# Performance work log

Hardware: AMD Instinct MI355X
Metric: run time of the kernel (lower is better)

## Reference

```python
import jax, jax.numpy as jnp
import numpy as np

N = 100000   # nodes
E = 1600000  # edges
D_IN = 4
D_H = 128
EPS = 1e-5

def setup_inputs() -> dict:
    key = jax.random.key(0)
    ks = jax.random.split(key, 4)
    x = jax.random.normal(ks[0], (N, D_IN), dtype=jnp.float32)
    edge_index = jax.random.randint(ks[1], (2, E), 0, N, dtype=jnp.int32)
    W0 = jax.random.normal(ks[2], (D_IN, D_H), dtype=jnp.float32) * 0.5
    b0 = jnp.zeros((D_H,), jnp.float32)
    W12 = jax.random.normal(ks[3], (2, D_H, D_H), dtype=jnp.float32) * (1.0 / np.sqrt(D_H))
    b12 = jnp.zeros((2, D_H), jnp.float32)
    gamma = jnp.ones((3, D_H), jnp.float32)   # GraphNorm weight
    beta = jnp.zeros((3, D_H), jnp.float32)   # GraphNorm bias
    alpha = jnp.ones((3, D_H), jnp.float32)   # GraphNorm mean_scale
    return dict(x=x, edge_index=edge_index, W0=W0, b0=b0, W12=W12, b12=b12,
                gamma=gamma, beta=beta, alpha=alpha)

def gcn_conv(x, src, dst, dinv, W, b):
    # PyG GCNConv: linear first, then D^-1/2 (A+I) D^-1/2 aggregation, bias after.
    h = x @ W                                  # [N, d_out]
    coef = dinv[src] * dinv[dst]               # [E]
    msg = h[src] * coef[:, None]               # [E, d_out] gather
    agg = jax.ops.segment_sum(msg, dst, num_segments=N)  # scatter-add
    agg = agg + h * (dinv * dinv)[:, None]     # self-loop contribution
    return agg + b

def graph_norm(x, g, be, a):
    # single-graph GraphNorm: gamma*(x - alpha*mu)/sqrt(E[(x-alpha*mu)^2]+eps)+beta
    mu = x.mean(axis=0)
    xc = x - a * mu
    var = (xc * xc).mean(axis=0)
    return g * xc * jax.lax.rsqrt(var + EPS) + be

def reference(x, edge_index, W0, b0, W12, b12, gamma, beta, alpha):
    src, dst = edge_index[0], edge_index[1]
    # degree with self loops (edge weight 1)
    deg = jax.ops.segment_sum(jnp.ones((E,), x.dtype), dst, num_segments=N) + 1.0
    dinv = jax.lax.rsqrt(deg)
    h = jax.nn.relu(graph_norm(gcn_conv(x, src, dst, dinv, W0, b0),
                               gamma[0], beta[0], alpha[0]))
    for i in range(2):  # fixed small layer loop
        h = jax.nn.relu(graph_norm(gcn_conv(h, src, dst, dinv, W12[i], b12[i]),
                                   gamma[i + 1], beta[i + 1], alpha[i + 1]))
    return h
```

## Files before the change

kernel.cpp:

```cpp
#include <hip/hip_runtime.h>


#define EPS_GN 1e-5f

typedef __attribute__((ext_vector_type(8))) _Float16 f16x8;
typedef __attribute__((ext_vector_type(2))) _Float16 f16x2;
typedef __attribute__((ext_vector_type(4))) float f32x4;

template <typename T, typename U>
__device__ __forceinline__ T bc(U u) {
  return __builtin_bit_cast(T, u);
}
__device__ __forceinline__ unsigned pkh(float x, float y) {
  return bc<unsigned>(__builtin_amdgcn_cvt_pkrtz(x, y));
}


__global__ __launch_bounds__(256) void k_count_p(const int* __restrict__ dst,
                                                 int* __restrict__ cnt, int E, int N) {
  int p = blockIdx.x & 7;
  int lo = (int)((long long)N * p >> 3), hi = (int)((long long)N * (p + 1) >> 3);
  int stride = (gridDim.x >> 3) * 256;
  for (int e = (blockIdx.x >> 3) * 256 + threadIdx.x; e < E; e += stride) {
    int d = dst[e];
    if (d >= lo && d < hi) atomicAdd(&cnt[d], 1);
  }
}

__global__ __launch_bounds__(256) void k_scan1(const int* __restrict__ cnt,
                                               int* __restrict__ rs,
                                               int* __restrict__ bsum, int N) {
  __shared__ int s[256];
  int t = threadIdx.x;
  int base = blockIdx.x * 1024 + t * 4;
  int c0 = (base + 0 < N) ? ((cnt[base + 0] + 8) & ~7) : 0;
  int c1 = (base + 1 < N) ? ((cnt[base + 1] + 8) & ~7) : 0;
  int c2 = (base + 2 < N) ? ((cnt[base + 2] + 8) & ~7) : 0;
  int c3 = (base + 3 < N) ? ((cnt[base + 3] + 8) & ~7) : 0;
  int tsum = c0 + c1 + c2 + c3;
  s[t] = tsum;
  __syncthreads();
  for (int off = 1; off < 256; off <<= 1) {
    int v = (t >= off) ? s[t - off] : 0;
    __syncthreads();
    s[t] += v;
    __syncthreads();
  }
  int excl = s[t] - tsum;
  if (t == 255) bsum[blockIdx.x] = s[255];
  int e0 = excl, e1 = e0 + c0, e2 = e1 + c1, e3 = e2 + c2;
  if (base + 0 < N) rs[base + 0] = e0;
  if (base + 1 < N) rs[base + 1] = e1;
  if (base + 2 < N) rs[base + 2] = e2;
  if (base + 3 < N) rs[base + 3] = e3;
}

__global__ __launch_bounds__(256) void k_scan2(const int* __restrict__ bsum,
                                               int* __restrict__ boff, int nblk) {
  __shared__ int s[256];
  int t = threadIdx.x;
  int v0 = (t < nblk) ? bsum[t] : 0;
  s[t] = v0;
  __syncthreads();
  for (int off = 1; off < 256; off <<= 1) {
    int v = (t >= off) ? s[t - off] : 0;
    __syncthreads();
    s[t] += v;
    __syncthreads();
  }
  if (t < nblk) boff[t] = s[t] - v0;
}

__global__ __launch_bounds__(256) void k_finalize(const int* __restrict__ cnt,
                                                  const int* __restrict__ boff,
                                                  int* __restrict__ rs,
                                                  int* __restrict__ cursor,
                                                  float* __restrict__ dinv,
                                                  unsigned* __restrict__ Hcb,
                                                  int* __restrict__ csrp, int N, int E,
                                                  int ROWS) {
  __shared__ int sTail;
  int i = blockIdx.x * 256 + threadIdx.x;
  int NB = N * 32;
  if (i < 64) Hcb[((size_t)(i >> 3) * ROWS + N) * 8 + (i & 7)] = 0u;
  if (i < N) {
    int v = rs[i] + boff[i >> 10];
    int c = cnt[i];
    int pc = (c + 8) & ~7;
    rs[i] = v;
    cursor[i] = v + 1;
    dinv[i] = rsqrtf((float)c + 1.0f);
    csrp[v] = i * 32;
    for (int k = v + 1 + c; k < v + pc; ++k) csrp[k] = NB;
    if (i == N - 1) {
      rs[N] = v + pc;
      sTail = v + pc;
    }
  }
  __syncthreads();
  if (blockIdx.x == gridDim.x - 1) {
    int base = sTail;
    for (int k = threadIdx.x; k < 1024; k += 256) csrp[base + k] = NB;
  }
}

__global__ __launch_bounds__(256) void k_fill_p(const int* __restrict__ src,
                                                const int* __restrict__ dst,
                                                int* __restrict__ cursor,
                                                int* __restrict__ csrp, int E, int N) {
  int p = blockIdx.x & 7;
  int lo = (int)((long long)N * p >> 3), hi = (int)((long long)N * (p + 1) >> 3);
  int stride = (gridDim.x >> 3) * 256;
  for (int e = (blockIdx.x >> 3) * 256 + threadIdx.x; e < E; e += stride) {
    int d = dst[e];
    if (d >= lo && d < hi) {
      int pos = atomicAdd(&cursor[d], 1);
      csrp[pos] = src[e] << 5;
    }
  }
}


__global__ __launch_bounds__(256) void k_wt(const float* __restrict__ W12,
                                            _Float16* __restrict__ WbT) {
  int o = blockIdx.x * 256 + threadIdx.x;
  int layer = o >> 14, r = o & 16383;
  int n = r >> 7, k = r & 127;
  WbT[o] = (_Float16)W12[layer * 16384 + k * 128 + n];
}


__global__ __launch_bounds__(256) void k_gemm0(const float* __restrict__ X,
                                               const float* __restrict__ W,
                                               const float* __restrict__ dinv,
                                               unsigned* __restrict__ Hcb, int N, int ROWS) {
  __shared__ float Ws[4 * 128];
  int t = threadIdx.x;
  if (t < 128) {
    Ws[t] = W[t];
    Ws[128 + t] = W[128 + t];
    Ws[256 + t] = W[256 + t];
    Ws[384 + t] = W[384 + t];
  }
  __syncthreads();
  int r = t >> 6, l = t & 63;
  int row = blockIdx.x * 4 + r;
  if (row >= N) return;
  float4 xv = ((const float4*)X)[row];
  float di = dinv[row];
  int c0 = 2 * l, c1 = 2 * l + 1;
  float v0 = xv.x * Ws[c0] + xv.y * Ws[128 + c0] + xv.z * Ws[256 + c0] + xv.w * Ws[384 + c0];
  float v1 = xv.x * Ws[c1] + xv.y * Ws[128 + c1] + xv.z * Ws[256 + c1] + xv.w * Ws[384 + c1];
  Hcb[((size_t)(l >> 3) * ROWS + row) * 8 + (l & 7)] = pkh(di * v0, di * v1);
}

__global__ __launch_bounds__(256, 4) void k_gemm_mfma(const unsigned* __restrict__ AGGcb,
                                                      const _Float16* __restrict__ WbT,
                                                      const float* __restrict__ stats,
                                                      const float* __restrict__ bias,
                                                      const float* __restrict__ gamma,
                                                      const float* __restrict__ beta,
                                                      const float* __restrict__ alpha,
                                                      const float* __restrict__ dinv,
                                                      unsigned* __restrict__ Hcb, int N,
                                                      int ROWS, float invN) {
  __shared__ float As[128], Bs[128];
  int t = threadIdx.x;
  if (t < 128) {
    float s1 = stats[t] * invN, s2 = stats[128 + t] * invN;
    float b = bias[t], a = alpha[t], g = gamma[t], be = beta[t];
    float mu = s1 + b;
    float E2 = s2 + 2.f * b * s1 + b * b;
    float var = E2 - (2.f * a - a * a) * mu * mu;
    float A = g * rsqrtf(var + EPS_GN);
    As[t] = A;
    Bs[t] = be - A * a * mu + A * b;
  }
  __syncthreads();
  int wv = t >> 6, l = t & 63;
  int r0 = blockIdx.x * 64 + wv * 16;
  if (r0 >= N) return;
  int m = l & 15, kb = l >> 4;

  f32x4 acc[8];
#pragma unroll
  for (int nt = 0; nt < 8; ++nt) acc[nt] = (f32x4){0.f, 0.f, 0.f, 0.f};

#pragma unroll
  for (int ks = 0; ks < 4; ++ks) {
    int k0 = ks * 32 + kb * 8;
    const uint4* pa = (const uint4*)(AGGcb + ((size_t)(2 * ks + (kb >> 1)) * ROWS + r0 + m) * 8 +
                                     (kb & 1) * 4);
    uint4 a_raw = pa[0];
    float4 A0 = *reinterpret_cast<const float4*>(&As[k0]);
    float4 A1 = *reinterpret_cast<const float4*>(&As[k0 + 4]);
    float4 B0 = *reinterpret_cast<const float4*>(&Bs[k0]);
    float4 B1 = *reinterpret_cast<const float4*>(&Bs[k0 + 4]);
    f16x8 bf[8];
#pragma unroll
    for (int nt = 0; nt < 8; ++nt)
      bf[nt] = *reinterpret_cast<const f16x8*>(WbT + (size_t)(nt * 16 + m) * 128 + k0);
    unsigned uu[4] = {a_raw.x, a_raw.y, a_raw.z, a_raw.w};
    float xr[8];
#pragma unroll
    for (int i = 0; i < 4; ++i) {
      f16x2 hp = bc<f16x2>(uu[i]);
      xr[2 * i] = (float)hp[0];
      xr[2 * i + 1] = (float)hp[1];
    }
    float Aa[8] = {A0.x, A0.y, A0.z, A0.w, A1.x, A1.y, A1.z, A1.w};
    float Bb[8] = {B0.x, B0.y, B0.z, B0.w, B1.x, B1.y, B1.z, B1.w};
    float xs[8];
#pragma unroll
    for (int j = 0; j < 8; ++j) {
      float v = fmaf(Aa[j], xr[j], Bb[j]);
      xs[j] = v > 0.f ? v : 0.f;
    }
    uint4 au;
    au.x = pkh(xs[0], xs[1]);
    au.y = pkh(xs[2], xs[3]);
    au.z = pkh(xs[4], xs[5]);
    au.w = pkh(xs[6], xs[7]);
    f16x8 af = bc<f16x8>(au);
#pragma unroll
    for (int nt = 0; nt < 8; ++nt)
      acc[nt] = __builtin_amdgcn_mfma_f32_16x16x32_f16(af, bf[nt], acc[nt], 0, 0, 0);
  }

  float dn[4];
#pragma unroll
  for (int r = 0; r < 4; ++r) dn[r] = dinv[r0 + kb * 4 + r];
  bool even = (l & 1) == 0;
#pragma unroll
  for (int nt = 0; nt < 8; ++nt) {
#pragma unroll
    for (int r = 0; r < 4; ++r) {
      float v = acc[nt][r] * dn[r];
      float pv = __shfl_xor(v, 1);
      if (even) {
        unsigned word = pkh(v, pv);
        Hcb[((size_t)nt * ROWS + r0 + kb * 4 + r) * 8 + (m >> 1)] = word;
      }
    }
  }
}

__global__ __launch_bounds__(256) void k_gather_cb(const unsigned* __restrict__ Hcb,
                                                   const int* __restrict__ rsp,
                                                   const int* __restrict__ csrp,
                                                   const float* __restrict__ dinv,
                                                   unsigned* __restrict__ AGGcb,
                                                   float* __restrict__ stats, int N, int ROWS) {
  int t = threadIdx.x;
  int wave = t >> 6, lane = t & 63;
  int g = lane >> 4, e = (lane >> 1) & 7, h = lane & 1;
  int p = blockIdx.x & 7;
  const unsigned char* HpB = (const unsigned char*)Hcb + (size_t)p * ROWS * 32;
  uint4* Ap4 = (uint4*)(AGGcb + (size_t)p * ROWS * 8);
  int NB = N * 32;
  int ho = h * 16;
  int q = blockIdx.x >> 3;
  int nstride = (gridDim.x >> 3) * 16;
  float s1acc[8], s2acc[8];
#pragma unroll
  for (int i = 0; i < 8; ++i) s1acc[i] = s2acc[i] = 0.f;

  for (int n0 = (q * 4 + wave) * 4; n0 < N; n0 += nstride) {
    int n = n0 + g;
    int j0 = rsp[n], j1 = rsp[n + 1];
    int nb = (j1 - j0) >> 3;
    int ml = nb;
    ml = max(ml, __shfl_xor(ml, 16));
    ml = max(ml, __shfl_xor(ml, 32));
    f16x2 acc[4];
#pragma unroll
    for (int i = 0; i < 4; ++i) acc[i] = (f16x2){(_Float16)0, (_Float16)0};

    const int* cp = csrp + j0 + e;
    auto hload = [&](int c, int b) -> uint4 {
      int ce = (b < nb) ? c : NB;
      return *(const uint4*)(HpB + (unsigned)(ce + ho));
    };
    int c0 = cp[0], c1 = cp[8];
    uint4 hA = hload(c0, 0);
    uint4 hB = hload(c1, 1);
    int c2 = cp[16], c3 = cp[24];
    const int* cpp = cp + 32;

    for (int b = 0; b < ml; b += 2) {
      acc[0] += bc<f16x2>(hA.x);
      acc[1] += bc<f16x2>(hA.y);
      acc[2] += bc<f16x2>(hA.z);
      acc[3] += bc<f16x2>(hA.w);
      hA = hload(c2, b + 2);
      c2 = cpp[0];
      if (b + 1 < ml) {
        acc[0] += bc<f16x2>(hB.x);
        acc[1] += bc<f16x2>(hB.y);
        acc[2] += bc<f16x2>(hB.z);
        acc[3] += bc<f16x2>(hB.w);
        hB = hload(c3, b + 3);
        c3 = cpp[8];
      }
      cpp += 16;
    }
#pragma unroll
    for (int i = 0; i < 4; ++i) {
      acc[i] += bc<f16x2>((unsigned)__shfl_xor(bc<int>(acc[i]), 2));
      acc[i] += bc<f16x2>((unsigned)__shfl_xor(bc<int>(acc[i]), 4));
      acc[i] += bc<f16x2>((unsigned)__shfl_xor(bc<int>(acc[i]), 8));
    }
    if (e == 0) {
      float dn = dinv[n];
      float v[8];
#pragma unroll
      for (int i = 0; i < 4; ++i) {
        v[2 * i] = (float)acc[i][0] * dn;
        v[2 * i + 1] = (float)acc[i][1] * dn;
      }
      uint4 wv;
      unsigned* wp = (unsigned*)&wv;
#pragma unroll
      for (int i = 0; i < 4; ++i) wp[i] = pkh(v[2 * i], v[2 * i + 1]);
      Ap4[(size_t)n * 2 + h] = wv;
#pragma unroll
      for (int i = 0; i < 8; ++i) {
        s1acc[i] += v[i];
        s2acc[i] = fmaf(v[i], v[i], s2acc[i]);
      }
    }
  }
#pragma unroll
  for (int i = 0; i < 8; ++i) {
    s1acc[i] += __shfl_xor(s1acc[i], 16);
    s1acc[i] += __shfl_xor(s1acc[i], 32);
    s2acc[i] += __shfl_xor(s2acc[i], 16);
    s2acc[i] += __shfl_xor(s2acc[i], 32);
  }
  __shared__ float sh[4][32];
  if (lane < 2) {
#pragma unroll
    for (int i = 0; i < 8; ++i) {
      sh[wave][h * 8 + i] = s1acc[i];
      sh[wave][16 + h * 8 + i] = s2acc[i];
    }
  }
  __syncthreads();
  if (t < 32) {
    float v = sh[0][t] + sh[1][t] + sh[2][t] + sh[3][t];
    if (t < 16)
      atomicAdd(&stats[p * 16 + t], v);
    else
      atomicAdd(&stats[128 + p * 16 + (t - 16)], v);
  }
}

__global__ __launch_bounds__(256) void k_norm(const unsigned* __restrict__ AGGcb,
                                              const float* __restrict__ stats,
                                              const float* __restrict__ bias,
                                              const float* __restrict__ gamma,
                                              const float* __restrict__ beta,
                                              const float* __restrict__ alpha,
                                              float* __restrict__ OUT, int N, int ROWS,
                                              float invN) {
  int i = blockIdx.x * 256 + threadIdx.x;
  if (i >= N * 32) return;
  int row = i >> 5, c4 = i & 31;
  int blk = c4 >> 2, off = (2 * c4) & 7;
  uint2 u = *(const uint2*)(AGGcb + ((size_t)blk * ROWS + row) * 8 + off);
  f16x2 p0 = bc<f16x2>(u.x), p1 = bc<f16x2>(u.y);
  float vv[4] = {(float)p0[0], (float)p0[1], (float)p1[0], (float)p1[1]};
  float ov[4];
#pragma unroll
  for (int j = 0; j < 4; ++j) {
    int c = c4 * 4 + j;
    float s1 = stats[c] * invN, s2 = stats[128 + c] * invN;
    float b = bias[c], a = alpha[c], g = gamma[c], be = beta[c];
    float mu = s1 + b;
    float E2 = s2 + 2.f * b * s1 + b * b;
    float var = E2 - (2.f * a - a * a) * mu * mu;
    float A = g * rsqrtf(var + EPS_GN);
    float B = be - A * a * mu + A * b;
    float o = fmaf(A, vv[j], B);
    ov[j] = o > 0.f ? o : 0.f;
  }
  ((float4*)OUT)[i] = make_float4(ov[0], ov[1], ov[2], ov[3]);
}


extern "C" void kernel_launch(void* const* d_in, const int* in_sizes, int n_in,
                              void* d_out, int out_size, void* d_ws, size_t ws_size,
                              hipStream_t stream) {
  const float* x = (const float*)d_in[0];
  const int* ei = (const int*)d_in[1];
  const float* W0 = (const float*)d_in[2];
  const float* b0 = (const float*)d_in[3];
  const float* W12 = (const float*)d_in[4];
  const float* b12 = (const float*)d_in[5];
  const float* gamma = (const float*)d_in[6];
  const float* beta = (const float*)d_in[7];
  const float* alpha = (const float*)d_in[8];
  float* out = (float*)d_out;

  int N = in_sizes[0] / 4;
  int E = in_sizes[1] / 2;
  int ROWS = N + 1;
  const int* srcArr = ei;
  const int* dstArr = ei + E;

  char* w = (char*)d_ws;
  auto alloc = [&](size_t bytes) {
    char* p = w;
    w += (bytes + 255) & ~(size_t)255;
    return p;
  };
  int* cnt = (int*)alloc((size_t)N * 4);
  float* stats = (float*)alloc(3 * 256 * 4);
  int* rs = (int*)alloc(((size_t)N + 1) * 4);
  int* cursor = (int*)alloc((size_t)N * 4);
  int* bsum = (int*)alloc(512);
  int* boff = (int*)alloc(512);
  _Float16* WbT = (_Float16*)alloc(2 * 16384 * 2);
  int* csrp = (int*)alloc(((size_t)E + 8 * (size_t)N + 2048) * 4);
  float* dinv = (float*)alloc((size_t)N * 4);
  unsigned* Hcb = (unsigned*)alloc((size_t)ROWS * 64 * 4);
  unsigned* AGGcb = (unsigned*)alloc((size_t)ROWS * 64 * 4);

  size_t zlen = (size_t)((char*)stats - (char*)cnt) + 3 * 256 * 4;
  hipMemsetAsync(cnt, 0, zlen, stream);

  int nblk = (N + 1023) / 1024;
  k_wt<<<128, 256, 0, stream>>>(W12, WbT);
  k_count_p<<<2048, 256, 0, stream>>>(dstArr, cnt, E, N);
  k_scan1<<<nblk, 256, 0, stream>>>(cnt, rs, bsum, N);
  k_scan2<<<1, 256, 0, stream>>>(bsum, boff, nblk);
  k_finalize<<<(N + 255) / 256, 256, 0, stream>>>(cnt, boff, rs, cursor, dinv, Hcb, csrp, N, E,
                                                  ROWS);
  k_fill_p<<<2048, 256, 0, stream>>>(srcArr, dstArr, cursor, csrp, E, N);

  float invN = 1.0f / (float)N;
  int gGemm = (N + 63) / 64;

  k_gemm0<<<(N + 3) / 4, 256, 0, stream>>>(x, W0, dinv, Hcb, N, ROWS);
  k_gather_cb<<<2048, 256, 0, stream>>>(Hcb, rs, csrp, dinv, AGGcb, stats, N, ROWS);
  k_gemm_mfma<<<gGemm, 256, 0, stream>>>(AGGcb, WbT, stats, b0, gamma, beta, alpha, dinv, Hcb, N,
                                         ROWS, invN);
  k_gather_cb<<<2048, 256, 0, stream>>>(Hcb, rs, csrp, dinv, AGGcb, stats + 256, N, ROWS);
  k_gemm_mfma<<<gGemm, 256, 0, stream>>>(AGGcb, WbT + 16384, stats + 256, b12, gamma + 128,
                                         beta + 128, alpha + 128, dinv, Hcb, N, ROWS, invN);
  k_gather_cb<<<2048, 256, 0, stream>>>(Hcb, rs, csrp, dinv, AGGcb, stats + 512, N, ROWS);
  k_norm<<<(N * 32 + 255) / 256, 256, 0, stream>>>(AGGcb, stats + 512, b12 + 128, gamma + 256,
                                                   beta + 256, alpha + 256, out, N, ROWS, invN);
}
```

Before: 609.8 us.

## Pad CSR rows to quad-max degree and unroll gather with uniform trip count

Each group of four nodes now gets the same padded CSR row length, set by the largest degree in the quad, so every wave handling those four nodes shares one loop bound taken via readfirstlane instead of a max-reduction over shuffles and per-lane bound checks. The gather loop is unrolled four-deep with four row loads in flight and index prefetching, aiming to raise memory-level parallelism. Rows padded with dummy entries point at a zero row, which adds wasted gather traffic for low-degree nodes and enlarges the CSR buffer.

```diff
diff --git a/kernel.cpp b/kernel.cpp
--- a/kernel.cpp
+++ b/kernel.cpp
@@ -33,11 +33,14 @@
   __shared__ int s[256];
   int t = threadIdx.x;
   int base = blockIdx.x * 1024 + t * 4;
-  int c0 = (base + 0 < N) ? ((cnt[base + 0] + 8) & ~7) : 0;
-  int c1 = (base + 1 < N) ? ((cnt[base + 1] + 8) & ~7) : 0;
-  int c2 = (base + 2 < N) ? ((cnt[base + 2] + 8) & ~7) : 0;
-  int c3 = (base + 3 < N) ? ((cnt[base + 3] + 8) & ~7) : 0;
-  int tsum = c0 + c1 + c2 + c3;
+  bool valid = base < N;
+  int c0 = valid ? cnt[base + 0] : 0;
+  int c1 = valid ? cnt[base + 1] : 0;
+  int c2 = valid ? cnt[base + 2] : 0;
+  int c3 = valid ? cnt[base + 3] : 0;
+  int mc = max(max(c0, c1), max(c2, c3));
+  int pcq = valid ? ((mc + 8) & ~7) : 0;
+  int tsum = pcq * 4;
   s[t] = tsum;
   __syncthreads();
   for (int off = 1; off < 256; off <<= 1) {
@@ -48,11 +51,12 @@
   }
   int excl = s[t] - tsum;
   if (t == 255) bsum[blockIdx.x] = s[255];
-  int e0 = excl, e1 = e0 + c0, e2 = e1 + c1, e3 = e2 + c2;
-  if (base + 0 < N) rs[base + 0] = e0;
-  if (base + 1 < N) rs[base + 1] = e1;
-  if (base + 2 < N) rs[base + 2] = e2;
-  if (base + 3 < N) rs[base + 3] = e3;
+  if (valid) {
+    rs[base + 0] = excl;
+    rs[base + 1] = excl + pcq;
+    rs[base + 2] = excl + 2 * pcq;
+    rs[base + 3] = excl + 3 * pcq;
+  }
 }
 
 __global__ __launch_bounds__(256) void k_scan2(const int* __restrict__ bsum,
@@ -84,9 +88,11 @@
   int NB = N * 32;
   if (i < 64) Hcb[((size_t)(i >> 3) * ROWS + N) * 8 + (i & 7)] = 0u;
   if (i < N) {
+    int qb = i & ~3;
+    int mc = max(max(cnt[qb], cnt[qb + 1]), max(cnt[qb + 2], cnt[qb + 3]));
+    int pc = (mc + 8) & ~7;
+    int c = cnt[i];
     int v = rs[i] + boff[i >> 10];
-    int c = cnt[i];
-    int pc = (c + 8) & ~7;
     rs[i] = v;
     cursor[i] = v + 1;
     dinv[i] = rsqrtf((float)c + 1.0f);
@@ -257,7 +263,6 @@
   int p = blockIdx.x & 7;
   const unsigned char* HpB = (const unsigned char*)Hcb + (size_t)p * ROWS * 32;
   uint4* Ap4 = (uint4*)(AGGcb + (size_t)p * ROWS * 8);
-  int NB = N * 32;
   int ho = h * 16;
   int q = blockIdx.x >> 3;
   int nstride = (gridDim.x >> 3) * 16;
@@ -267,42 +272,63 @@
 
   for (int n0 = (q * 4 + wave) * 4; n0 < N; n0 += nstride) {
     int n = n0 + g;
-    int j0 = rsp[n], j1 = rsp[n + 1];
-    int nb = (j1 - j0) >> 3;
-    int ml = nb;
-    ml = max(ml, __shfl_xor(ml, 16));
-    ml = max(ml, __shfl_xor(ml, 32));
+    int j0 = rsp[n];
+    int nb = __builtin_amdgcn_readfirstlane((rsp[n + 1] - j0) >> 3);
     f16x2 acc[4];
 #pragma unroll
     for (int i = 0; i < 4; ++i) acc[i] = (f16x2){(_Float16)0, (_Float16)0};
 
     const int* cp = csrp + j0 + e;
-    auto hload = [&](int c, int b) -> uint4 {
-      int ce = (b < nb) ? c : NB;
-      return *(const uint4*)(HpB + (unsigned)(ce + ho));
-    };
-    int c0 = cp[0], c1 = cp[8];
-    uint4 hA = hload(c0, 0);
-    uint4 hB = hload(c1, 1);
-    int c2 = cp[16], c3 = cp[24];
-    const int* cpp = cp + 32;
-
-    for (int b = 0; b < ml; b += 2) {
-      acc[0] += bc<f16x2>(hA.x);
-      acc[1] += bc<f16x2>(hA.y);
-      acc[2] += bc<f16x2>(hA.z);
-      acc[3] += bc<f16x2>(hA.w);
-      hA = hload(c2, b + 2);
-      c2 = cpp[0];
-      if (b + 1 < ml) {
-        acc[0] += bc<f16x2>(hB.x);
-        acc[1] += bc<f16x2>(hB.y);
-        acc[2] += bc<f16x2>(hB.z);
-        acc[3] += bc<f16x2>(hB.w);
-        hB = hload(c3, b + 3);
-        c3 = cpp[8];
-      }
-      cpp += 16;
+    auto ldh = [&](int c) -> uint4 { return *(const uint4*)(HpB + (unsigned)(c + ho)); };
+
+    uint4 h0 = ldh(cp[0]);
+    uint4 h1 = {}, h2 = {}, h3 = {};
+    if (nb > 1) h1 = ldh(cp[8]);
+    if (nb > 2) h2 = ldh(cp[16]);
+    if (nb > 3) h3 = ldh(cp[24]);
+    int cA = 0, cB = 0, cC = 0, cD = 0;
+    if (nb > 4) {
+      cA = cp[32];
+      cB = cp[40];
+      cC = cp[48];
+      cD = cp[56];
+    }
+    const int* cpn = cp + 64;
+
+    for (int b = 0; b < nb; b += 4) {
+      acc[0] += bc<f16x2>(h0.x);
+      acc[1] += bc<f16x2>(h0.y);
+      acc[2] += bc<f16x2>(h0.z);
+      acc[3] += bc<f16x2>(h0.w);
+      if (b + 4 < nb) h0 = ldh(cA);
+      if (b + 1 < nb) {
+        acc[0] += bc<f16x2>(h1.x);
+        acc[1] += bc<f16x2>(h1.y);
+        acc[2] += bc<f16x2>(h1.z);
+        acc[3] += bc<f16x2>(h1.w);
+        if (b + 5 < nb) h1 = ldh(cB);
+      }
+      if (b + 2 < nb) {
+        acc[0] += bc<f16x2>(h2.x);
+        acc[1] += bc<f16x2>(h2.y);
+        acc[2] += bc<f16x2>(h2.z);
+        acc[3] += bc<f16x2>(h2.w);
+        if (b + 6 < nb) h2 = ldh(cC);
+      }
+      if (b + 3 < nb) {
+        acc[0] += bc<f16x2>(h3.x);
+        acc[1] += bc<f16x2>(h3.y);
+        acc[2] += bc<f16x2>(h3.z);
+        acc[3] += bc<f16x2>(h3.w);
+        if (b + 7 < nb) h3 = ldh(cD);
+      }
+      if (b + 8 < nb) {
+        cA = cpn[0];
+        cB = cpn[8];
+        cC = cpn[16];
+        cD = cpn[24];
+      }
+      cpn += 32;
     }
 #pragma unroll
     for (int i = 0; i < 4; ++i) {
@@ -421,7 +447,7 @@
   int* bsum = (int*)alloc(512);
   int* boff = (int*)alloc(512);
   _Float16* WbT = (_Float16*)alloc(2 * 16384 * 2);
-  int* csrp = (int*)alloc(((size_t)E + 8 * (size_t)N + 2048) * 4);
+  int* csrp = (int*)alloc(((size_t)E + 24 * (size_t)N + 2048) * 4);
   float* dinv = (float*)alloc((size_t)N * 4);
   unsigned* Hcb = (unsigned*)alloc((size_t)ROWS * 64 * 4);
   unsigned* AGGcb = (unsigned*)alloc((size_t)ROWS * 64 * 4);
```

Result: slower. 680.1 us (+11.5%).
